# Optimization experiments

Measured on AMD Instinct MI355X. Metric: run time of the kernel, lower is better.

The kernel has to match this reference:

```python
import jax, jax.numpy as jnp
import numpy as np

FG_FRACTION = 0.5
BATCHSIZE = 256
NUM_IMAGES = 1
NUM_CLASSES = 21
FG_THRESH = 0.5
BG_THRESH_HI = 0.5
BG_THRESH_LO = 0.1
ROIS_PER_IMAGE = BATCHSIZE // NUM_IMAGES                      # 256
FG_ROIS_PER_IMAGE = int(round(FG_FRACTION * ROIS_PER_IMAGE))  # 128
BG_ROIS_PER_IMAGE = ROIS_PER_IMAGE - FG_ROIS_PER_IMAGE        # 128


def _make_boxes(key, n, img=1000.0, max_wh=200.0):
    k1, k2 = jax.random.split(key)
    xy = jax.random.uniform(k1, (n, 2), dtype=jnp.float32) * (img - max_wh)
    wh = jax.random.uniform(k2, (n, 2), dtype=jnp.float32) * max_wh + 1.0
    return jnp.concatenate([xy, xy + wh], axis=1)  # valid [x1,y1,x2,y2]


def setup_inputs() -> dict:
    key = jax.random.key(0)
    k1, k2, k3 = jax.random.split(key, 3)
    N, G = 250000, 128
    rois = _make_boxes(k1, N)
    all_rois = jnp.concatenate([jnp.zeros((N, 1), jnp.float32), rois], axis=1)  # [N,5], col0 = image idx
    gt_boxes = _make_boxes(k2, G)                                               # [G,4]
    gt_labels = jax.random.randint(k3, (G,), 1, NUM_CLASSES).astype(jnp.int32)  # fg classes 1..20
    return {"all_rois": all_rois, "gt_boxes": gt_boxes, "gt_labels": gt_labels}


def _iou(a, b):
    area_a = (a[:, 2] - a[:, 0] + 1.0) * (a[:, 3] - a[:, 1] + 1.0)
    area_b = (b[:, 2] - b[:, 0] + 1.0) * (b[:, 3] - b[:, 1] + 1.0)
    ix1 = jnp.maximum(a[:, None, 0], b[None, :, 0])
    iy1 = jnp.maximum(a[:, None, 1], b[None, :, 1])
    ix2 = jnp.minimum(a[:, None, 2], b[None, :, 2])
    iy2 = jnp.minimum(a[:, None, 3], b[None, :, 3])
    iw = jnp.clip(ix2 - ix1 + 1.0, 0.0)
    ih = jnp.clip(iy2 - iy1 + 1.0, 0.0)
    inter = iw * ih
    return inter / (area_a[:, None] + area_b[None, :] - inter)


def _bbox_transform(ex, gt):
    ew = ex[:, 2] - ex[:, 0] + 1.0
    eh = ex[:, 3] - ex[:, 1] + 1.0
    ecx = ex[:, 0] + 0.5 * ew
    ecy = ex[:, 1] + 0.5 * eh
    gw = gt[:, 2] - gt[:, 0] + 1.0
    gh = gt[:, 3] - gt[:, 1] + 1.0
    gcx = gt[:, 0] + 0.5 * gw
    gcy = gt[:, 1] + 0.5 * gh
    return jnp.stack([(gcx - ecx) / ew, (gcy - ecy) / eh,
                      jnp.log(gw / ew), jnp.log(gh / eh)], axis=1)


def _proposal_target(all_rois, gt_boxes, gt_labels):
    G = gt_boxes.shape[0]
    # append gt boxes (with image-index 0 column) to the proposal set
    gt_rois = jnp.concatenate([jnp.zeros((G, 1), all_rois.dtype), gt_boxes], axis=1)
    all_rois = jnp.concatenate([all_rois, gt_rois], axis=0)          # [N+G, 5]

    overlaps = _iou(all_rois[:, 1:5], gt_boxes)                       # [N+G, G] -- dominant memory traffic
    gt_assignment = jnp.argmax(overlaps, axis=1)                      # [N+G]
    max_ov = jnp.max(overlaps, axis=1)                                # [N+G]
    labels_all = gt_labels[gt_assignment]                             # [N+G]

    fg_mask = max_ov >= FG_THRESH
    bg_mask = (max_ov < BG_THRESH_HI) & (max_ov >= BG_THRESH_LO)

    # random fg/bg sampling: top-k over random keys restricted to each mask
    u = jax.random.uniform(jax.random.key(42), (all_rois.shape[0],), dtype=jnp.float32)
    fg_idx = jax.lax.top_k(jnp.where(fg_mask, u, -1.0), FG_ROIS_PER_IMAGE)[1]
    bg_idx = jax.lax.top_k(jnp.where(bg_mask, u, -1.0), BG_ROIS_PER_IMAGE)[1]
    keep = jnp.concatenate([fg_idx, bg_idx])                          # [256]

    valid_fg = fg_mask[fg_idx]  # if fewer fg than requested, pad slots get label 0
    labels = jnp.concatenate([jnp.where(valid_fg, labels_all[fg_idx], 0),
                              jnp.zeros((BG_ROIS_PER_IMAGE,), labels_all.dtype)])

    rois = all_rois[keep]                                             # [256, 5]
    targets = _bbox_transform(rois[:, 1:5], gt_boxes[gt_assignment[keep]])  # [256, 4]

    # scatter targets into class-specific columns [256, 4*num_classes]
    onehot = jax.nn.one_hot(labels, NUM_CLASSES, dtype=targets.dtype)
    bbox_targets = (onehot[:, :, None] * targets[:, None, :]).reshape(ROIS_PER_IMAGE, 4 * NUM_CLASSES)
    bbox_targets = bbox_targets * (labels > 0)[:, None].astype(targets.dtype)
    return rois, labels, bbox_targets


def reference(all_rois, gt_boxes, gt_labels):
    return _proposal_target(all_rois, gt_boxes, gt_labels)
```

## Files before the change

### kernel.cpp

```cpp
#include <hip/hip_runtime.h>
#include <stdint.h>

#define GMAX 128
#define TK 128
#define NBINS 4096
#define CAND_MAX 4096
#define NUM_CLASSES 21

typedef float f32x4u __attribute__((ext_vector_type(4), aligned(4)));

__device__ __forceinline__ void threefry2x32(uint32_t k0, uint32_t k1,
                                             uint32_t& x0, uint32_t& x1) {
  uint32_t ks0 = k0, ks1 = k1, ks2 = k0 ^ k1 ^ 0x1BD11BDAu;
  x0 += ks0; x1 += ks1;
#define TF_ROUND(r) { x0 += x1; x1 = (x1 << (r)) | (x1 >> (32 - (r))); x1 ^= x0; }
  TF_ROUND(13) TF_ROUND(15) TF_ROUND(26) TF_ROUND(6)
  x0 += ks1; x1 += ks2 + 1u;
  TF_ROUND(17) TF_ROUND(29) TF_ROUND(16) TF_ROUND(24)
  x0 += ks2; x1 += ks0 + 2u;
  TF_ROUND(13) TF_ROUND(15) TF_ROUND(26) TF_ROUND(6)
  x0 += ks0; x1 += ks1 + 3u;
  TF_ROUND(17) TF_ROUND(29) TF_ROUND(16) TF_ROUND(24)
  x0 += ks1; x1 += ks2 + 4u;
  TF_ROUND(13) TF_ROUND(15) TF_ROUND(26) TF_ROUND(6)
  x0 += ks2; x1 += ks0 + 5u;
#undef TF_ROUND
}

__global__ void __launch_bounds__(256)
score_kernel(const float* __restrict__ all_rois,
             const float* __restrict__ gt_boxes,
             uint32_t* __restrict__ score,
             uint32_t* __restrict__ hist,
             int* __restrict__ meta,
             int N, int M, int G) {
  const int t = threadIdx.x;
  const int i = blockIdx.x * 256 + t;
  const bool active = (i < M);

  float bx1 = 0.0f, by1 = 0.0f, bx2 = 0.0f, by2 = 0.0f;
  if (active) {
    if (i < N) {
      f32x4u v = *reinterpret_cast<const f32x4u*>(all_rois + (size_t)i * 5 + 1);
      bx1 = v.x; by1 = v.y; bx2 = v.z; by2 = v.w;
    } else {
      float4 b = reinterpret_cast<const float4*>(gt_boxes)[i - N];
      bx1 = b.x; by1 = b.y; bx2 = b.z; by2 = b.w;
    }
  }
  const float area = __fmul_rn(__fadd_rn(__fsub_rn(bx2, bx1), 1.0f),
                               __fadd_rn(__fsub_rn(by2, by1), 1.0f));
  float best = -1.0f;
  int bi = 0;
  const float4* __restrict__ gt4 = reinterpret_cast<const float4*>(gt_boxes);
#pragma unroll 8
  for (int g = 0; g < GMAX; ++g) {
    const float4 gb = gt4[g];
    float ga = __fmul_rn(__fadd_rn(__fsub_rn(gb.z, gb.x), 1.0f),
                         __fadd_rn(__fsub_rn(gb.w, gb.y), 1.0f));
    float ix1 = fmaxf(bx1, gb.x);
    float iy1 = fmaxf(by1, gb.y);
    float ix2 = fminf(bx2, gb.z);
    float iy2 = fminf(by2, gb.w);
    float iw = fmaxf(__fadd_rn(__fsub_rn(ix2, ix1), 1.0f), 0.0f);
    float ih = fmaxf(__fadd_rn(__fsub_rn(iy2, iy1), 1.0f), 0.0f);
    float inter = __fmul_rn(iw, ih);
    float uni = __fsub_rn(__fadd_rn(area, ga), inter);
    float ov = __fdiv_rn(inter, uni);
    if (ov > best) { best = ov; bi = g; }
  }

  if (active) {
    uint32_t cx0 = 0u, cx1 = (uint32_t)i;
    threefry2x32(0u, 42u, cx0, cx1);
    uint32_t ubits = (cx0 ^ cx1) >> 9;
    uint32_t fg = (best >= 0.5f) ? 1u : 0u;
    uint32_t bg = (!fg && best >= 0.1f) ? 1u : 0u;
    score[i] = (ubits << 9) | ((uint32_t)bi << 2) | (fg << 1) | bg;
    if (fg)      atomicAdd(&hist[ubits >> 11], 1u);
    else if (bg) atomicAdd(&hist[NBINS + (ubits >> 11)], 1u);
  }

  asm volatile("s_waitcnt vmcnt(0)" ::: "memory");
  __syncthreads();
  __shared__ unsigned s_prev;
  if (t == 0) s_prev = atomicAdd((unsigned int*)&meta[2], 1u);
  __syncthreads();
  if (s_prev != gridDim.x - 1) return;

  __shared__ uint64_t gs[256];
  __shared__ int s_jstar[2];
  const int b0 = 16 * t;
  uint64_t acc = 0;
  for (int k = 0; k < 16; ++k) {
    uint32_t hf = __hip_atomic_load(&hist[b0 + k], __ATOMIC_RELAXED,
                                    __HIP_MEMORY_SCOPE_AGENT);
    uint32_t hb = __hip_atomic_load(&hist[NBINS + b0 + k], __ATOMIC_RELAXED,
                                    __HIP_MEMORY_SCOPE_AGENT);
    acc += ((uint64_t)hf << 32) | (uint64_t)hb;
  }
  gs[t] = acc;
  if (t < 2) s_jstar[t] = -1;
  __syncthreads();
  for (int d = 1; d < 256; d <<= 1) {
    uint64_t add = (t + d < 256) ? gs[t + d] : 0ull;
    __syncthreads();
    gs[t] += add;
    __syncthreads();
  }
  uint32_t vfg = (uint32_t)(gs[t] >> 32);
  uint32_t vbg = (uint32_t)gs[t];
  uint32_t nfg = (t < 255) ? (uint32_t)(gs[t + 1] >> 32) : 0u;
  uint32_t nbg = (t < 255) ? (uint32_t)gs[t + 1] : 0u;
  if (vfg >= (uint32_t)TK && (t == 255 || nfg < (uint32_t)TK)) s_jstar[0] = t;
  if (vbg >= (uint32_t)TK && (t == 255 || nbg < (uint32_t)TK)) s_jstar[1] = t;
  __syncthreads();
  if (t == 0) {
    for (int m = 0; m < 2; ++m) {
      int j = s_jstar[m], B = -1;
      if (j >= 0) {
        uint32_t base = 0;
        if (j < 255)
          base = (m == 0) ? (uint32_t)(gs[j + 1] >> 32) : (uint32_t)gs[j + 1];
        B = 16 * j;
        for (int b = 16 * j + 15; b >= 16 * j; --b) {
          base += __hip_atomic_load(&hist[m * NBINS + b], __ATOMIC_RELAXED,
                                    __HIP_MEMORY_SCOPE_AGENT);
          if (base >= (uint32_t)TK) { B = b; break; }
        }
      }
      meta[4 + m] = B;
    }
  }
}

__global__ void __launch_bounds__(256)
compact_kernel(const uint32_t* __restrict__ score, int M,
               int* __restrict__ meta,
               uint64_t* __restrict__ cand) {
  const int bth[2] = {meta[4], meta[5]};
  const int base = (blockIdx.x * 256 + threadIdx.x) * 4;
  if (base >= M) return;
  uint32_t ss[4];
  int lim;
  if (base + 3 < M) {
    uint4 s4 = *reinterpret_cast<const uint4*>(score + base);
    ss[0] = s4.x; ss[1] = s4.y; ss[2] = s4.z; ss[3] = s4.w;
    lim = 4;
  } else {
    lim = M - base;
    for (int k = 0; k < lim; ++k) ss[k] = score[base + k];
  }
  for (int k = 0; k < lim; ++k) {
    uint32_t s = ss[k];
    uint32_t mb = s & 3u;
    if (!mb) continue;
    int m = (mb & 2u) ? 0 : 1;
    int B = bth[m];
    if (B >= 0 && (int)(s >> 20) < B) continue;
    int p = atomicAdd(&meta[m], 1);
    if (p < CAND_MAX)
      cand[(size_t)m * CAND_MAX + p] =
          (((uint64_t)((s >> 9) + 1u)) << 32) | (uint64_t)(~(uint32_t)(base + k));
  }
}

__global__ void __launch_bounds__(1024)
final_kernel(const float* __restrict__ all_rois,
             const float* __restrict__ gt_boxes,
             const int* __restrict__ gt_labels,
             const uint32_t* __restrict__ score,
             const uint64_t* __restrict__ cand_g,
             const int* __restrict__ meta,
             float* __restrict__ out, int N, int M) {
  __shared__ uint64_t cand[CAND_MAX];
  __shared__ int keep[2 * TK];
  __shared__ int fgvalid[TK];
  __shared__ float s_tx[2 * TK], s_ty[2 * TK], s_tw[2 * TK], s_th[2 * TK];
  __shared__ int s_label[2 * TK];
  const int t = threadIdx.x;

  for (int m = 0; m < 2; ++m) {
    int cnt = meta[m]; if (cnt > CAND_MAX) cnt = CAND_MAX;
    for (int p = t; p < cnt; p += 1024)
      cand[p] = cand_g[(size_t)m * CAND_MAX + p];
    __syncthreads();
    for (int p = t; p < cnt; p += 1024) {
      uint64_t key = cand[p];
      int r = 0;
      for (int j = 0; j < cnt; ++j) r += (cand[j] > key) ? 1 : 0;
      if (r < TK) {
        keep[m * TK + r] = (int)(~(uint32_t)(key & 0xFFFFFFFFull));
        if (m == 0) fgvalid[r] = 1;
      }
    }
    __syncthreads();
    if (cnt < TK && t == 0) {
      int fill = cnt;
      uint32_t mask_bit = (m == 0) ? 2u : 1u;
      for (int i2 = 0; i2 < M && fill < TK; ++i2)
        if (!(score[i2] & mask_bit)) {
          keep[m * TK + fill] = i2;
          if (m == 0) fgvalid[fill] = 0;
          fill++;
        }
    }
    __syncthreads();
  }

  const int R = 2 * TK;
  float* rois_out   = out;
  float* labels_out = out + (size_t)R * 5;
  float* bt_out     = out + (size_t)R * 5 + R;

  if (t < R) {
    const int i = keep[t];
    float rimg, rx1, ry1, rx2, ry2;
    if (i < N) {
      rimg = all_rois[(size_t)i * 5 + 0];
      rx1  = all_rois[(size_t)i * 5 + 1];
      ry1  = all_rois[(size_t)i * 5 + 2];
      rx2  = all_rois[(size_t)i * 5 + 3];
      ry2  = all_rois[(size_t)i * 5 + 4];
    } else {
      int g = i - N;
      rimg = 0.0f;
      rx1 = gt_boxes[g * 4 + 0]; ry1 = gt_boxes[g * 4 + 1];
      rx2 = gt_boxes[g * 4 + 2]; ry2 = gt_boxes[g * 4 + 3];
    }
    rois_out[t * 5 + 0] = rimg;
    rois_out[t * 5 + 1] = rx1;
    rois_out[t * 5 + 2] = ry1;
    rois_out[t * 5 + 3] = rx2;
    rois_out[t * 5 + 4] = ry2;

    const int ga = (int)((score[i] >> 2) & 127u);
    int label = (t < TK && fgvalid[t]) ? gt_labels[ga] : 0;
    labels_out[t] = (float)label;
    s_label[t] = label;

    float gx1 = gt_boxes[ga * 4 + 0], gy1 = gt_boxes[ga * 4 + 1];
    float gx2 = gt_boxes[ga * 4 + 2], gy2 = gt_boxes[ga * 4 + 3];
    float ew = rx2 - rx1 + 1.0f, eh = ry2 - ry1 + 1.0f;
    float ecx = rx1 + 0.5f * ew, ecy = ry1 + 0.5f * eh;
    float gw = gx2 - gx1 + 1.0f, gh = gy2 - gy1 + 1.0f;
    float gcx = gx1 + 0.5f * gw, gcy = gy1 + 0.5f * gh;
    s_tx[t] = (gcx - ecx) / ew;
    s_ty[t] = (gcy - ecy) / eh;
    s_tw[t] = logf(gw / ew);
    s_th[t] = logf(gh / eh);
  }
  __syncthreads();

  const int TOT = R * 4 * NUM_CLASSES;
  for (int idx = t; idx < TOT; idx += 1024) {
    int r = idx / (4 * NUM_CLASSES);
    int c = idx - r * (4 * NUM_CLASSES);
    int lab = s_label[r];
    float v = 0.0f;
    if (lab > 0 && (c >> 2) == lab) {
      int cc = c & 3;
      v = (cc == 0) ? s_tx[r] : (cc == 1) ? s_ty[r] : (cc == 2) ? s_tw[r] : s_th[r];
    }
    bt_out[idx] = v;
  }
}

extern "C" void kernel_launch(void* const* d_in, const int* in_sizes, int n_in,
                              void* d_out, int out_size, void* d_ws, size_t ws_size,
                              hipStream_t stream) {
  const float* all_rois = (const float*)d_in[0];
  const float* gt_boxes = (const float*)d_in[1];
  const int*   gt_labels = (const int*)d_in[2];
  const int N = in_sizes[0] / 5;
  const int G = in_sizes[2];
  const int M = N + G;

  char* ws = (char*)d_ws;
  int* meta = (int*)ws;
  uint32_t* hist = (uint32_t*)(ws + 256);
  size_t off = 256 + (size_t)2 * NBINS * 4;
  uint32_t* score = (uint32_t*)(ws + off);
  off += (((size_t)M * 4) + 255) & ~(size_t)255;
  uint64_t* cand = (uint64_t*)(ws + off);
  float* out = (float*)d_out;

  hipMemsetAsync(ws, 0, 256 + (size_t)2 * NBINS * 4, stream);
  score_kernel<<<(M + 255) / 256, 256, 0, stream>>>(all_rois, gt_boxes, score,
                                                    hist, meta, N, M, G);
  const int nb4 = ((M + 3) / 4 + 255) / 256;
  compact_kernel<<<nb4, 256, 0, stream>>>(score, M, meta, cand);
  final_kernel<<<1, 1024, 0, stream>>>(all_rois, gt_boxes, gt_labels, score,
                                       cand, meta, out, N, M);
}
```

Baseline: 115.7 us.

## Split IoU argmax across four lanes per ROI with shuffle reduction

```diff
diff --git a/kernel.cpp b/kernel.cpp
--- a/kernel.cpp
+++ b/kernel.cpp
@@ -34,8 +34,18 @@
              uint32_t* __restrict__ hist,
              int* __restrict__ meta,
              int N, int M, int G) {
+  __shared__ float sga[132];
   const int t = threadIdx.x;
-  const int i = blockIdx.x * 256 + t;
+  if (t < 128) {
+    float4 b = reinterpret_cast<const float4*>(gt_boxes)[t];
+    sga[t + (t >> 5)] = __fmul_rn(__fadd_rn(__fsub_rn(b.z, b.x), 1.0f),
+                                  __fadd_rn(__fsub_rn(b.w, b.y), 1.0f));
+  }
+  __syncthreads();
+
+  const int gid = blockIdx.x * 256 + t;
+  const int i = gid >> 2;
+  const int q = gid & 3;
   const bool active = (i < M);
 
   float bx1 = 0.0f, by1 = 0.0f, bx2 = 0.0f, by2 = 0.0f;
@@ -53,11 +63,11 @@
   float best = -1.0f;
   int bi = 0;
   const float4* __restrict__ gt4 = reinterpret_cast<const float4*>(gt_boxes);
-#pragma unroll 8
-  for (int g = 0; g < GMAX; ++g) {
-    const float4 gb = gt4[g];
-    float ga = __fmul_rn(__fadd_rn(__fsub_rn(gb.z, gb.x), 1.0f),
-                         __fadd_rn(__fsub_rn(gb.w, gb.y), 1.0f));
+  const int g0 = q * 32;
+#pragma unroll 4
+  for (int g = 0; g < 32; ++g) {
+    const float4 gb = gt4[g0 + g];
+    const float ga = sga[g0 + g + q];
     float ix1 = fmaxf(bx1, gb.x);
     float iy1 = fmaxf(by1, gb.y);
     float ix2 = fminf(bx2, gb.z);
@@ -67,10 +77,20 @@
     float inter = __fmul_rn(iw, ih);
     float uni = __fsub_rn(__fadd_rn(area, ga), inter);
     float ov = __fdiv_rn(inter, uni);
-    if (ov > best) { best = ov; bi = g; }
-  }
-
-  if (active) {
+    if (ov > best) { best = ov; bi = g0 + g; }
+  }
+
+  unsigned long long key =
+      ((unsigned long long)__float_as_uint(best) << 32) |
+      (unsigned long long)(uint32_t)(127 - bi);
+  unsigned long long o = __shfl_xor(key, 1, 64);
+  key = (o > key) ? o : key;
+  o = __shfl_xor(key, 2, 64);
+  key = (o > key) ? o : key;
+  best = __uint_as_float((uint32_t)(key >> 32));
+  bi = 127 - (int)(key & 127ull);
+
+  if (active && q == 0) {
     uint32_t cx0 = 0u, cx1 = (uint32_t)i;
     threefry2x32(0u, 42u, cx0, cx1);
     uint32_t ubits = (cx0 ^ cx1) >> 9;
@@ -286,8 +306,10 @@
   float* out = (float*)d_out;
 
   hipMemsetAsync(ws, 0, 256 + (size_t)2 * NBINS * 4, stream);
-  score_kernel<<<(M + 255) / 256, 256, 0, stream>>>(all_rois, gt_boxes, score,
-                                                    hist, meta, N, M, G);
+  const long long nthreads = (long long)M * 4;
+  const int nblocks = (int)((nthreads + 255) / 256);
+  score_kernel<<<nblocks, 256, 0, stream>>>(all_rois, gt_boxes, score,
+                                            hist, meta, N, M, G);
   const int nb4 = ((M + 3) / 4 + 255) / 256;
   compact_kernel<<<nb4, 256, 0, stream>>>(score, M, meta, cand);
   final_kernel<<<1, 1024, 0, stream>>>(all_rois, gt_boxes, gt_labels, score,
```

New measurement: 156.7 us. 35.5% more time.

## Split GT loop across four waves per ROI and fuse compact with final stage

Applied to the files above, without the earlier changes.

```diff
diff --git a/kernel.cpp b/kernel.cpp
--- a/kernel.cpp
+++ b/kernel.cpp
@@ -34,8 +34,11 @@
              uint32_t* __restrict__ hist,
              int* __restrict__ meta,
              int N, int M, int G) {
+  __shared__ uint64_t lds_key[256];
   const int t = threadIdx.x;
-  const int i = blockIdx.x * 256 + t;
+  const int lane = t & 63;
+  const int w = __builtin_amdgcn_readfirstlane(t >> 6);
+  const int i = blockIdx.x * 64 + lane;
   const bool active = (i < M);
 
   float bx1 = 0.0f, by1 = 0.0f, bx2 = 0.0f, by2 = 0.0f;
@@ -53,9 +56,10 @@
   float best = -1.0f;
   int bi = 0;
   const float4* __restrict__ gt4 = reinterpret_cast<const float4*>(gt_boxes);
+  const int g0 = w * 32;
 #pragma unroll 8
-  for (int g = 0; g < GMAX; ++g) {
-    const float4 gb = gt4[g];
+  for (int g = 0; g < 32; ++g) {
+    const float4 gb = gt4[g0 + g];
     float ga = __fmul_rn(__fadd_rn(__fsub_rn(gb.z, gb.x), 1.0f),
                          __fadd_rn(__fsub_rn(gb.w, gb.y), 1.0f));
     float ix1 = fmaxf(bx1, gb.x);
@@ -67,18 +71,34 @@
     float inter = __fmul_rn(iw, ih);
     float uni = __fsub_rn(__fadd_rn(area, ga), inter);
     float ov = __fdiv_rn(inter, uni);
-    if (ov > best) { best = ov; bi = g; }
-  }
-
-  if (active) {
-    uint32_t cx0 = 0u, cx1 = (uint32_t)i;
-    threefry2x32(0u, 42u, cx0, cx1);
-    uint32_t ubits = (cx0 ^ cx1) >> 9;
-    uint32_t fg = (best >= 0.5f) ? 1u : 0u;
-    uint32_t bg = (!fg && best >= 0.1f) ? 1u : 0u;
-    score[i] = (ubits << 9) | ((uint32_t)bi << 2) | (fg << 1) | bg;
-    if (fg)      atomicAdd(&hist[ubits >> 11], 1u);
-    else if (bg) atomicAdd(&hist[NBINS + (ubits >> 11)], 1u);
+    if (ov > best) { best = ov; bi = g0 + g; }
+  }
+
+  lds_key[t] = ((uint64_t)__float_as_uint(best) << 32) |
+               (uint64_t)(uint32_t)(127 - bi);
+  __syncthreads();
+
+  if (t < 64) {
+    uint64_t k0 = lds_key[t];
+    uint64_t k1 = lds_key[64 + t];
+    uint64_t k2 = lds_key[128 + t];
+    uint64_t k3 = lds_key[192 + t];
+    uint64_t kk = (k1 > k0) ? k1 : k0;
+    kk = (k2 > kk) ? k2 : kk;
+    kk = (k3 > kk) ? k3 : kk;
+    best = __uint_as_float((uint32_t)(kk >> 32));
+    bi = 127 - (int)(kk & 127ull);
+
+    if (active) {
+      uint32_t cx0 = 0u, cx1 = (uint32_t)i;
+      threefry2x32(0u, 42u, cx0, cx1);
+      uint32_t ubits = (cx0 ^ cx1) >> 9;
+      uint32_t fg = (best >= 0.5f) ? 1u : 0u;
+      uint32_t bg = (!fg && best >= 0.1f) ? 1u : 0u;
+      score[i] = (ubits << 9) | ((uint32_t)bi << 2) | (fg << 1) | bg;
+      if (fg)      atomicAdd(&hist[ubits >> 11], 1u);
+      else if (bg) atomicAdd(&hist[NBINS + (ubits >> 11)], 1u);
+    }
   }
 
   asm volatile("s_waitcnt vmcnt(0)" ::: "memory");
@@ -135,57 +155,68 @@
 }
 
 __global__ void __launch_bounds__(256)
-compact_kernel(const uint32_t* __restrict__ score, int M,
-               int* __restrict__ meta,
-               uint64_t* __restrict__ cand) {
-  const int bth[2] = {meta[4], meta[5]};
-  const int base = (blockIdx.x * 256 + threadIdx.x) * 4;
-  if (base >= M) return;
-  uint32_t ss[4];
-  int lim;
-  if (base + 3 < M) {
-    uint4 s4 = *reinterpret_cast<const uint4*>(score + base);
-    ss[0] = s4.x; ss[1] = s4.y; ss[2] = s4.z; ss[3] = s4.w;
-    lim = 4;
-  } else {
-    lim = M - base;
-    for (int k = 0; k < lim; ++k) ss[k] = score[base + k];
-  }
-  for (int k = 0; k < lim; ++k) {
-    uint32_t s = ss[k];
-    uint32_t mb = s & 3u;
-    if (!mb) continue;
-    int m = (mb & 2u) ? 0 : 1;
-    int B = bth[m];
-    if (B >= 0 && (int)(s >> 20) < B) continue;
-    int p = atomicAdd(&meta[m], 1);
-    if (p < CAND_MAX)
-      cand[(size_t)m * CAND_MAX + p] =
-          (((uint64_t)((s >> 9) + 1u)) << 32) | (uint64_t)(~(uint32_t)(base + k));
-  }
-}
-
-__global__ void __launch_bounds__(1024)
-final_kernel(const float* __restrict__ all_rois,
-             const float* __restrict__ gt_boxes,
-             const int* __restrict__ gt_labels,
-             const uint32_t* __restrict__ score,
-             const uint64_t* __restrict__ cand_g,
-             const int* __restrict__ meta,
-             float* __restrict__ out, int N, int M) {
+compact_final_kernel(const float* __restrict__ all_rois,
+                     const float* __restrict__ gt_boxes,
+                     const int* __restrict__ gt_labels,
+                     const uint32_t* __restrict__ score, int M, int N,
+                     int* __restrict__ meta,
+                     uint64_t* __restrict__ cand_g,
+                     float* __restrict__ out) {
+  const int t = threadIdx.x;
+
+  {
+    const int bth[2] = {meta[4], meta[5]};
+    const int base = (blockIdx.x * 256 + t) * 4;
+    if (base < M) {
+      uint32_t ss[4];
+      int lim;
+      if (base + 3 < M) {
+        uint4 s4 = *reinterpret_cast<const uint4*>(score + base);
+        ss[0] = s4.x; ss[1] = s4.y; ss[2] = s4.z; ss[3] = s4.w;
+        lim = 4;
+      } else {
+        lim = M - base;
+        for (int k = 0; k < lim; ++k) ss[k] = score[base + k];
+      }
+      for (int k = 0; k < lim; ++k) {
+        uint32_t s = ss[k];
+        uint32_t mb = s & 3u;
+        if (!mb) continue;
+        int m = (mb & 2u) ? 0 : 1;
+        int B = bth[m];
+        if (B >= 0 && (int)(s >> 20) < B) continue;
+        int p = atomicAdd(&meta[m], 1);
+        if (p < CAND_MAX)
+          atomicExch((unsigned long long*)&cand_g[(size_t)m * CAND_MAX + p],
+                     (((uint64_t)((s >> 9) + 1u)) << 32) |
+                         (uint64_t)(~(uint32_t)(base + k)));
+      }
+    }
+  }
+
+  asm volatile("s_waitcnt vmcnt(0)" ::: "memory");
+  __syncthreads();
+  __shared__ unsigned s_prev;
+  if (t == 0) s_prev = atomicAdd((unsigned int*)&meta[3], 1u);
+  __syncthreads();
+  if (s_prev != gridDim.x - 1) return;
+
   __shared__ uint64_t cand[CAND_MAX];
   __shared__ int keep[2 * TK];
   __shared__ int fgvalid[TK];
   __shared__ float s_tx[2 * TK], s_ty[2 * TK], s_tw[2 * TK], s_th[2 * TK];
   __shared__ int s_label[2 * TK];
-  const int t = threadIdx.x;
 
   for (int m = 0; m < 2; ++m) {
-    int cnt = meta[m]; if (cnt > CAND_MAX) cnt = CAND_MAX;
-    for (int p = t; p < cnt; p += 1024)
-      cand[p] = cand_g[(size_t)m * CAND_MAX + p];
-    __syncthreads();
-    for (int p = t; p < cnt; p += 1024) {
+    int cnt = (int)__hip_atomic_load((unsigned int*)&meta[m], __ATOMIC_RELAXED,
+                                     __HIP_MEMORY_SCOPE_AGENT);
+    if (cnt > CAND_MAX) cnt = CAND_MAX;
+    for (int p = t; p < cnt; p += 256)
+      cand[p] = __hip_atomic_load(
+          (unsigned long long*)&cand_g[(size_t)m * CAND_MAX + p],
+          __ATOMIC_RELAXED, __HIP_MEMORY_SCOPE_AGENT);
+    __syncthreads();
+    for (int p = t; p < cnt; p += 256) {
       uint64_t key = cand[p];
       int r = 0;
       for (int j = 0; j < cnt; ++j) r += (cand[j] > key) ? 1 : 0;
@@ -213,7 +244,7 @@
   float* labels_out = out + (size_t)R * 5;
   float* bt_out     = out + (size_t)R * 5 + R;
 
-  if (t < R) {
+  {
     const int i = keep[t];
     float rimg, rx1, ry1, rx2, ry2;
     if (i < N) {
@@ -253,7 +284,7 @@
   __syncthreads();
 
   const int TOT = R * 4 * NUM_CLASSES;
-  for (int idx = t; idx < TOT; idx += 1024) {
+  for (int idx = t; idx < TOT; idx += 256) {
     int r = idx / (4 * NUM_CLASSES);
     int c = idx - r * (4 * NUM_CLASSES);
     int lab = s_label[r];
@@ -286,10 +317,10 @@
   float* out = (float*)d_out;
 
   hipMemsetAsync(ws, 0, 256 + (size_t)2 * NBINS * 4, stream);
-  score_kernel<<<(M + 255) / 256, 256, 0, stream>>>(all_rois, gt_boxes, score,
-                                                    hist, meta, N, M, G);
+  const int nblocks = (M + 63) / 64;
+  score_kernel<<<nblocks, 256, 0, stream>>>(all_rois, gt_boxes, score,
+                                            hist, meta, N, M, G);
   const int nb4 = ((M + 3) / 4 + 255) / 256;
-  compact_kernel<<<nb4, 256, 0, stream>>>(score, M, meta, cand);
-  final_kernel<<<1, 1024, 0, stream>>>(all_rois, gt_boxes, gt_labels, score,
-                                       cand, meta, out, N, M);
+  compact_final_kernel<<<nb4, 256, 0, stream>>>(all_rois, gt_boxes, gt_labels,
+                                                score, M, N, meta, cand, out);
 }
```

Measured after the change: 139.2 us. 20.3% more time.

## Cull IoU candidates with a uniform grid of GT-box bitmasks

Applied to the files above, without the earlier changes.

```diff
diff --git a/kernel.cpp b/kernel.cpp
--- a/kernel.cpp
+++ b/kernel.cpp
@@ -6,6 +6,8 @@
 #define NBINS 4096
 #define CAND_MAX 4096
 #define NUM_CLASSES 21
+#define NCELL 16
+#define CINV 0.015625f
 
 typedef float f32x4u __attribute__((ext_vector_type(4), aligned(4)));
 
@@ -27,53 +29,111 @@
 #undef TF_ROUND
 }
 
+__global__ void __launch_bounds__(512)
+prep_kernel(const float* __restrict__ gt_boxes,
+            uint32_t* __restrict__ hist, int* __restrict__ meta,
+            uint64_t* __restrict__ cellm) {
+  const int b = blockIdx.x, t = threadIdx.x;
+  if (b > 0) {
+    const int idx = (b - 1) * 512 + t;
+    if (idx < 2 * NBINS) hist[idx] = 0;
+    return;
+  }
+  if (t < 64) meta[t] = 0;
+  if (t < 256) {
+    const float4* __restrict__ gt4 = reinterpret_cast<const float4*>(gt_boxes);
+    const int cx = t & 15, cy = t >> 4;
+    const float x0 = cx * 64.0f, x1 = x0 + 64.0f;
+    const float y0 = cy * 64.0f, y1 = y0 + 64.0f;
+    uint64_t m0 = 0, m1 = 0;
+    for (int g = 0; g < GMAX; ++g) {
+      float4 gb = gt4[g];
+      bool ov = (gb.x - 2.0f <= x1) && (gb.z + 2.0f >= x0) &&
+                (gb.y - 2.0f <= y1) && (gb.w + 2.0f >= y0);
+      if (ov) { if (g < 64) m0 |= 1ull << g; else m1 |= 1ull << (g - 64); }
+    }
+    cellm[2 * t]     = m0;
+    cellm[2 * t + 1] = m1;
+  }
+}
+
 __global__ void __launch_bounds__(256)
 score_kernel(const float* __restrict__ all_rois,
              const float* __restrict__ gt_boxes,
+             const uint64_t* __restrict__ cellm,
              uint32_t* __restrict__ score,
              uint32_t* __restrict__ hist,
              int* __restrict__ meta,
-             int N, int M, int G) {
+             int N, int M) {
+  __shared__ float4 sbox[GMAX];
+  __shared__ float sga[GMAX];
+  __shared__ __align__(16) uint64_t scell[512];
   const int t = threadIdx.x;
+  const float4* __restrict__ gt4 = reinterpret_cast<const float4*>(gt_boxes);
+  if (t < GMAX) {
+    float4 b = gt4[t];
+    sbox[t] = b;
+    sga[t] = __fmul_rn(__fadd_rn(__fsub_rn(b.z, b.x), 1.0f),
+                       __fadd_rn(__fsub_rn(b.w, b.y), 1.0f));
+  }
+  scell[t]       = cellm[t];
+  scell[256 + t] = cellm[256 + t];
+  __syncthreads();
+
   const int i = blockIdx.x * 256 + t;
   const bool active = (i < M);
-
   float bx1 = 0.0f, by1 = 0.0f, bx2 = 0.0f, by2 = 0.0f;
   if (active) {
     if (i < N) {
       f32x4u v = *reinterpret_cast<const f32x4u*>(all_rois + (size_t)i * 5 + 1);
       bx1 = v.x; by1 = v.y; bx2 = v.z; by2 = v.w;
     } else {
-      float4 b = reinterpret_cast<const float4*>(gt_boxes)[i - N];
+      float4 b = sbox[i - N];
       bx1 = b.x; by1 = b.y; bx2 = b.z; by2 = b.w;
     }
   }
   const float area = __fmul_rn(__fadd_rn(__fsub_rn(bx2, bx1), 1.0f),
                                __fadd_rn(__fsub_rn(by2, by1), 1.0f));
-  float best = -1.0f;
+
+  uint64_t m0 = 0, m1 = 0;
+  if (active) {
+    int cx0 = (int)(bx1 * CINV), cx1 = (int)(bx2 * CINV);
+    int cy0 = (int)(by1 * CINV), cy1 = (int)(by2 * CINV);
+    if (cx1 > 15) cx1 = 15;
+    if (cy1 > 15) cy1 = 15;
+    for (int cy = cy0; cy <= cy1; ++cy)
+      for (int cx = cx0; cx <= cx1; ++cx) {
+        const int c = (cy << 4) + cx;
+        ulonglong2 p = *reinterpret_cast<const ulonglong2*>(&scell[2 * c]);
+        m0 |= p.x; m1 |= p.y;
+      }
+  }
+
+  float best = 0.0f;
   int bi = 0;
-  const float4* __restrict__ gt4 = reinterpret_cast<const float4*>(gt_boxes);
-#pragma unroll 8
-  for (int g = 0; g < GMAX; ++g) {
-    const float4 gb = gt4[g];
-    float ga = __fmul_rn(__fadd_rn(__fsub_rn(gb.z, gb.x), 1.0f),
-                         __fadd_rn(__fsub_rn(gb.w, gb.y), 1.0f));
-    float ix1 = fmaxf(bx1, gb.x);
-    float iy1 = fmaxf(by1, gb.y);
-    float ix2 = fminf(bx2, gb.z);
-    float iy2 = fminf(by2, gb.w);
-    float iw = fmaxf(__fadd_rn(__fsub_rn(ix2, ix1), 1.0f), 0.0f);
-    float ih = fmaxf(__fadd_rn(__fsub_rn(iy2, iy1), 1.0f), 0.0f);
-    float inter = __fmul_rn(iw, ih);
-    float uni = __fsub_rn(__fadd_rn(area, ga), inter);
-    float ov = __fdiv_rn(inter, uni);
-    if (ov > best) { best = ov; bi = g; }
-  }
+#define IOU_AT(gidx)                                                    \
+  {                                                                     \
+    float4 gb = sbox[gidx];                                             \
+    float ga = sga[gidx];                                               \
+    float ix1 = fmaxf(bx1, gb.x);                                       \
+    float iy1 = fmaxf(by1, gb.y);                                       \
+    float ix2 = fminf(bx2, gb.z);                                       \
+    float iy2 = fminf(by2, gb.w);                                       \
+    float iw = fmaxf(__fadd_rn(__fsub_rn(ix2, ix1), 1.0f), 0.0f);       \
+    float ih = fmaxf(__fadd_rn(__fsub_rn(iy2, iy1), 1.0f), 0.0f);       \
+    float inter = __fmul_rn(iw, ih);                                    \
+    float uni = __fsub_rn(__fadd_rn(area, ga), inter);                  \
+    float ov = __fdiv_rn(inter, uni);    \
+    if (ov > best) { best = ov; bi = (gidx); }                          \
+  }
+  while (m0) { int g = __builtin_ctzll(m0); m0 &= m0 - 1; IOU_AT(g); }
+  while (m1) { int g = 64 + __builtin_ctzll(m1); m1 &= m1 - 1; IOU_AT(g); }
+#undef IOU_AT
 
   if (active) {
-    uint32_t cx0 = 0u, cx1 = (uint32_t)i;
-    threefry2x32(0u, 42u, cx0, cx1);
-    uint32_t ubits = (cx0 ^ cx1) >> 9;
+    uint32_t c0 = 0u, c1 = (uint32_t)i;
+    threefry2x32(0u, 42u, c0, c1);
+    uint32_t ubits = (c0 ^ c1) >> 9;
     uint32_t fg = (best >= 0.5f) ? 1u : 0u;
     uint32_t bg = (!fg && best >= 0.1f) ? 1u : 0u;
     score[i] = (ubits << 9) | ((uint32_t)bi << 2) | (fg << 1) | bg;
@@ -275,6 +335,7 @@
   const int N = in_sizes[0] / 5;
   const int G = in_sizes[2];
   const int M = N + G;
+  (void)G;
 
   char* ws = (char*)d_ws;
   int* meta = (int*)ws;
@@ -283,11 +344,14 @@
   uint32_t* score = (uint32_t*)(ws + off);
   off += (((size_t)M * 4) + 255) & ~(size_t)255;
   uint64_t* cand = (uint64_t*)(ws + off);
+  off += (size_t)2 * CAND_MAX * 8;
+  uint64_t* cellm = (uint64_t*)(ws + off);
   float* out = (float*)d_out;
 
-  hipMemsetAsync(ws, 0, 256 + (size_t)2 * NBINS * 4, stream);
-  score_kernel<<<(M + 255) / 256, 256, 0, stream>>>(all_rois, gt_boxes, score,
-                                                    hist, meta, N, M, G);
+  prep_kernel<<<17, 512, 0, stream>>>(gt_boxes, hist, meta, cellm);
+  const int nblocks = (M + 255) / 256;
+  score_kernel<<<nblocks, 256, 0, stream>>>(all_rois, gt_boxes, cellm, score,
+                                            hist, meta, N, M);
   const int nb4 = ((M + 3) / 4 + 255) / 256;
   compact_kernel<<<nb4, 256, 0, stream>>>(score, M, meta, cand);
   final_kernel<<<1, 1024, 0, stream>>>(all_rois, gt_boxes, gt_labels, score,
```

Result: slower. 122.1 us (+5.5%).
